# Kernel tuning notes

Measured on AMD Instinct MI355X. Metric: run time of the kernel, lower is better.

Reference implementation:

```python
import jax, jax.numpy as jnp
import numpy as np

B, S, HID, H, DH = 4, 1024, 1024, 16, 64
MAX_REL = 16
SCALE = 1.0 / (DH ** 0.5)


def _rel_bias(emb, seq_len):
    # Shaw-style relative position bias: emb is [2*MAX_REL+1, DH]
    pos = jnp.arange(seq_len)
    dist = jnp.clip(pos[None, :] - pos[:, None], -MAX_REL, MAX_REL) + MAX_REL
    return emb[dist]  # [S, S, DH]


def setup_inputs() -> dict:
    key = jax.random.key(0)
    ks = jax.random.split(key, 14)
    n = jax.random.normal
    w = 0.02
    return {
        "query": n(ks[0], (B, S, HID), dtype=jnp.float32),
        "key": n(ks[1], (B, S, HID), dtype=jnp.float32),
        "value": n(ks[2], (B, S, HID), dtype=jnp.float32),
        # per-head projection weights stacked over heads
        "Wq": n(ks[3], (H, HID, DH), dtype=jnp.float32) * w,
        "bq": n(ks[4], (H, DH), dtype=jnp.float32) * w,
        "Wk": n(ks[5], (H, HID, DH), dtype=jnp.float32) * w,
        "bk": n(ks[6], (H, DH), dtype=jnp.float32) * w,
        "Wv": n(ks[7], (H, HID, DH), dtype=jnp.float32) * w,
        "bv": n(ks[8], (H, DH), dtype=jnp.float32) * w,
        # relative-position embedding tables (shared across heads)
        "rel_k_emb": n(ks[9], (2 * MAX_REL + 1, DH), dtype=jnp.float32) * w,
        "rel_v_emb": n(ks[10], (2 * MAX_REL + 1, DH), dtype=jnp.float32) * w,
        # output projection fc: Linear(hidden, hidden)
        "fc_W": n(ks[11], (HID, HID), dtype=jnp.float32) * w,
        "fc_b": n(ks[12], (HID,), dtype=jnp.float32) * w,
    }


def reference(query, key, value, Wq, bq, Wk, bk, Wv, bv, rel_k_emb, rel_v_emb, fc_W, fc_b):
    # per-head projections, all heads batched: [B, H, S, DH]
    q = jnp.einsum('bsd,hde->bhse', query, Wq) + bq[None, :, None, :]
    k = jnp.einsum('bsd,hde->bhse', key, Wk) + bk[None, :, None, :]
    v = jnp.einsum('bsd,hde->bhse', value, Wv) + bv[None, :, None, :]

    k_bias = _rel_bias(rel_k_emb, S)  # [S, S, DH]
    v_bias = _rel_bias(rel_v_emb, S)  # [S, S, DH]

    # scores: QK^T plus relative-position key bias term
    scores = jnp.einsum('bhqe,bhke->bhqk', q, k)
    scores = scores + jnp.einsum('bhqe,qke->bhqk', q, k_bias)
    attn = jax.nn.softmax(scores * SCALE, axis=-1)  # [B, H, S, S]

    # values: A V plus relative-position value bias term
    out = jnp.einsum('bhqk,bhke->bhqe', attn, v)
    out = out + jnp.einsum('bhqk,qke->bhqe', attn, v_bias)

    # concat heads -> [B, S, HID], then fc
    out = out.transpose(0, 2, 1, 3).reshape(B, S, HID)
    return out @ fc_W.T + fc_b
```

## Files before the change

kernel.cpp:

```cpp
#include <hip/hip_runtime.h>
#include <stdint.h>

#define B_ 4
#define S_ 1024
#define HID_ 1024
#define H_ 16
#define DH_ 64
#define NDIST 33
#define SCALE_ 0.125f

typedef unsigned short u16;
typedef __attribute__((ext_vector_type(8))) short short8;
typedef __attribute__((ext_vector_type(4))) float floatx4;

static __device__ __forceinline__ float bf2f(u16 u) {
  union { unsigned int i; float f; } v; v.i = ((unsigned int)u) << 16; return v.f;
}
static __device__ __forceinline__ u16 f2bf(float x) {
  union { float f; unsigned int i; } v; v.f = x;
  return (u16)((v.i + 0x7FFFu + ((v.i >> 16) & 1u)) >> 16);
}
static __device__ __forceinline__ floatx4 mfma_bf16(short8 a, short8 b, floatx4 c) {
  return __builtin_amdgcn_mfma_f32_16x16x32_bf16(a, b, c, 0, 0, 0);
}
static __device__ __forceinline__ void gload_lds16(const void* g, void* l) {
  __builtin_amdgcn_global_load_lds(
      (const __attribute__((address_space(1))) unsigned int*)g,
      (__attribute__((address_space(3))) unsigned int*)l, 16, 0, 0);
}

#define OFF_BQ   0
#define OFF_BK   1024
#define OFF_BV   2048
#define OFF_RELK 3072
#define OFF_RELV 5184
#define OFF_FCW  7296
#define OFF_FCB  1055872
#define CONV_TOT 1056896

struct SrcPtrs { const void* p[7]; };

__global__ __launch_bounds__(256) void detect_kernel(const u16* __restrict__ q,
                                                     int* __restrict__ flag) {
  __shared__ float red[256];
  float m = 0.f;
  for (int i = threadIdx.x; i < 8192; i += 256) {
    float v = fabsf(bf2f(q[2 * i]));
    m = fmaxf(m, (v < 1e30f) ? v : 1e20f);
  }
  red[threadIdx.x] = m;
  __syncthreads();
  for (int s = 128; s > 0; s >>= 1) {
    if (threadIdx.x < (unsigned)s) red[threadIdx.x] = fmaxf(red[threadIdx.x], red[threadIdx.x + s]);
    __syncthreads();
  }
  if (threadIdx.x == 0) *flag = (red[0] > 1e4f) ? 1 : 0;
}

__global__ __launch_bounds__(256) void convert_kernel(SrcPtrs srcs,
                                                      const int* __restrict__ flag,
                                                      u16* __restrict__ dst) {
  constexpr int segsz[7] = {1024,1024,1024,2112,2112,1048576,1024};
  constexpr int cumE[7]  = {OFF_BQ,OFF_BK,OFF_BV,OFF_RELK,OFF_RELV,OFF_FCW,OFF_FCB};
  constexpr int cumB[8]  = {0,1,2,3,6,9,1033,1034};
  const int bid = blockIdx.x;
  int t = 0;
  #pragma unroll
  for (int i = 1; i < 7; ++i) if (bid >= cumB[i]) t = i;
  const int chunk = (bid - cumB[t]) * 1024 + threadIdx.x * 4;
  if (chunk >= segsz[t]) return;
  __align__(8) u16 o[4];
  if (*flag) {
    const float* s = (const float*)srcs.p[t];
    float4 v = *(const float4*)(s + chunk);
    o[0] = f2bf(v.x); o[1] = f2bf(v.y); o[2] = f2bf(v.z); o[3] = f2bf(v.w);
  } else {
    const u16* s = (const u16*)srcs.p[t];
    *(uint2*)o = *(const uint2*)(s + chunk);
  }
  *(uint2*)(dst + cumE[t] + chunk) = *(const uint2*)o;
}

__global__ __launch_bounds__(256) void wtrans_kernel(
    const void* __restrict__ Wq, const void* __restrict__ Wk, const void* __restrict__ Wv,
    const int* __restrict__ flag, u16* __restrict__ wt)
{
  const int dt = blockIdx.x, h = blockIdx.y, z = blockIdx.z;
  const void* W = (z == 0) ? Wq : (z == 1) ? Wk : Wv;
  const int tid = threadIdx.x;
  const int isf = *flag;
  __shared__ __align__(16) u16 t_l[64 * 72];

  #pragma unroll
  for (int i = 0; i < 2; ++i) {
    int g = tid + 256 * i;
    int d = g & 63, e8 = (g >> 6) * 8;
    size_t off = ((size_t)h * HID_ + dt * 64 + d) * DH_ + e8;
    __align__(16) u16 tmp[8];
    if (isf) {
      const float* Wf = (const float*)W + off;
      float4 v0 = *(const float4*)Wf;
      float4 v1 = *(const float4*)(Wf + 4);
      tmp[0]=f2bf(v0.x); tmp[1]=f2bf(v0.y); tmp[2]=f2bf(v0.z); tmp[3]=f2bf(v0.w);
      tmp[4]=f2bf(v1.x); tmp[5]=f2bf(v1.y); tmp[6]=f2bf(v1.z); tmp[7]=f2bf(v1.w);
    } else {
      *(uint4*)tmp = *(const uint4*)((const u16*)W + off);
    }
    #pragma unroll
    for (int j = 0; j < 8; ++j) {
      int e = e8 + j;
      t_l[e * 72 + (((d >> 3) ^ (e & 7)) << 3) + (d & 7)] = tmp[j];
    }
  }
  __syncthreads();
  {
    int e = tid >> 2, c0 = (tid & 3) * 2;
    u16* dst = wt + ((size_t)(z * H_ + h) * DH_ + e) * HID_ + dt * 64;
    uint4 x0 = *(const uint4*)(t_l + e * 72 + (((c0    ) ^ (e & 7)) << 3));
    uint4 x1 = *(const uint4*)(t_l + e * 72 + (((c0 + 1) ^ (e & 7)) << 3));
    *(uint4*)(dst + c0 * 8)     = x0;
    *(uint4*)(dst + c0 * 8 + 8) = x1;
  }
}

__global__ __launch_bounds__(256) void proj_kernel(
    const void* __restrict__ qin, const void* __restrict__ kin, const void* __restrict__ vin,
    const u16* __restrict__ wt, const u16* __restrict__ conv,
    const int* __restrict__ flag,
    u16* __restrict__ qo, u16* __restrict__ ko, u16* __restrict__ vo)
{
  const int z = blockIdx.z;
  const void* A   = (z == 0) ? qin : (z == 1) ? kin : vin;
  const u16* Wz   = wt + (size_t)z * (H_ * DH_ * HID_);
  const u16* bias = conv + ((z == 0) ? OFF_BQ : (z == 1) ? OFF_BK : OFF_BV);
  u16*       O    = (z == 0) ? qo : (z == 1) ? ko : vo;
  const int rt = blockIdx.x, ct = blockIdx.y;
  const int tid = threadIdx.x, lane = tid & 63, w = tid >> 6, quad = lane >> 4, l16 = lane & 15;
  const int isf = *flag;

  __shared__ __align__(16) u16 a_l[128 * 32];
  __shared__ __align__(16) u16 b_l[128 * 32];

  floatx4 acc[4][4];
  #pragma unroll
  for (int i = 0; i < 4; ++i)
    #pragma unroll
    for (int j = 0; j < 4; ++j) acc[i][j] = (floatx4){0.f,0.f,0.f,0.f};

  const int mq = (w & 1) * 64, nq = (w >> 1) * 64;

  for (int kk = 0; kk < 32; ++kk) {
    __syncthreads();
    #pragma unroll
    for (int i = 0; i < 2; ++i) {
      int idx = tid + 256 * i;
      int row = idx >> 2, c8 = (idx & 3) * 8;
      if (isf) {
        const float* Af = (const float*)A + (size_t)(rt * 128 + row) * HID_ + kk * 32 + c8;
        float4 v0 = *(const float4*)Af;
        float4 v1 = *(const float4*)(Af + 4);
        __align__(16) u16 tmp[8] = {f2bf(v0.x),f2bf(v0.y),f2bf(v0.z),f2bf(v0.w),
                                    f2bf(v1.x),f2bf(v1.y),f2bf(v1.z),f2bf(v1.w)};
        *(uint4*)(a_l + row * 32 + c8) = *(const uint4*)tmp;
      } else {
        *(uint4*)(a_l + row * 32 + c8) =
            *(const uint4*)((const u16*)A + (size_t)(rt * 128 + row) * HID_ + kk * 32 + c8);
      }
      gload_lds16(Wz + (size_t)(ct * 128 + row) * HID_ + kk * 32 + c8,
                  b_l + ((size_t)(w * 64 + i * 256)) * 8);
    }
    __syncthreads();
    short8 af[4], bfr[4];
    #pragma unroll
    for (int i = 0; i < 4; ++i) {
      af[i]  = *(const short8*)(a_l + (mq + i * 16 + l16) * 32 + quad * 8);
      bfr[i] = *(const short8*)(b_l + (nq + i * 16 + l16) * 32 + quad * 8);
    }
    #pragma unroll
    for (int i = 0; i < 4; ++i)
      #pragma unroll
      for (int j = 0; j < 4; ++j)
        acc[i][j] = mfma_bf16(af[i], bfr[j], acc[i][j]);
  }

  #pragma unroll
  for (int j = 0; j < 4; ++j) {
    int col = ct * 128 + nq + j * 16 + l16;
    int hh = col >> 6, e = col & 63;
    float bb = bf2f(bias[hh * 64 + e]);
    #pragma unroll
    for (int i = 0; i < 4; ++i) {
      #pragma unroll
      for (int r = 0; r < 4; ++r) {
        int m = rt * 128 + mq + i * 16 + quad * 4 + r;
        int bidx = m >> 10, srow = m & 1023;
        O[(((size_t)(bidx * H_ + hh)) * S_ + srow) * DH_ + e] = f2bf(acc[i][j][r] + bb);
      }
    }
  }
}

__global__ __launch_bounds__(256, 4) void attn_kernel(
    const u16* __restrict__ Q, const u16* __restrict__ K, const u16* __restrict__ V,
    const u16* __restrict__ conv, u16* __restrict__ Ox)
{
  const int bid = blockIdx.x + 16 * (blockIdx.y + 16 * blockIdx.z);
  const int nid = (bid & 7) * 128 + (bid >> 3);
  const int qt = nid & 15, h = (nid >> 4) & 15, b = nid >> 8;

  const int tid = threadIdx.x;
  const int lane = tid & 63, w = tid >> 6, quad = lane >> 4, l16 = lane & 15;
  const size_t base = ((size_t)(b * H_ + h)) * S_ * DH_;

  __shared__ __align__(16) char smem[40320];
  u16*   p_l    = (u16*)(smem);
  u16*   q_l    = p_l;
  u16*   k_l    = (u16*)(smem + 9216);
  u16*   vt_l   = (u16*)(smem + 18432);
  u16*   rq_l   = (u16*)(smem + 27648);
  float* bucket = (float*)(smem + 31872);
  u16*   rkb    = (u16*)(smem + 31872);

  #pragma unroll
  for (int i = 0; i < 2; ++i) {
    int idx = tid + 256 * i;
    int row = idx >> 3, c8 = (idx & 7) * 8;
    *(uint4*)(q_l + row * 72 + c8) =
        *(const uint4*)(Q + base + (size_t)(qt * 64 + row) * DH_ + c8);
  }
  const u16* relk = conv + OFF_RELK;
  for (int idx = tid; idx < 48 * 8; idx += 256) {
    int row = idx >> 3, c8 = (idx & 7) * 8;
    uint4 v = make_uint4(0, 0, 0, 0);
    if (row < NDIST) v = *(const uint4*)(relk + row * 64 + c8);
    *(uint4*)(rkb + row * 72 + c8) = v;
  }
  __syncthreads();

  const int m0 = w * 16;
  short8 qa0 = *(const short8*)(q_l + (m0 + l16) * 72 + quad * 8);
  short8 qa1 = *(const short8*)(q_l + (m0 + l16) * 72 + 32 + quad * 8);

  floatx4 c_d0 = {0.f,0.f,0.f,0.f}, c_d32 = {0.f,0.f,0.f,0.f};
  #pragma unroll
  for (int t3 = 0; t3 < 3; ++t3) {
    floatx4 c = {0.f,0.f,0.f,0.f};
    c = mfma_bf16(qa0, *(const short8*)(rkb + (t3 * 16 + l16) * 72 + quad * 8), c);
    c = mfma_bf16(qa1, *(const short8*)(rkb + (t3 * 16 + l16) * 72 + 32 + quad * 8), c);
    if (t3 == 0) c_d0 = c;
    if (t3 == 2) c_d32 = c;
    int d = t3 * 16 + l16;
    if (d < NDIST) {
      #pragma unroll
      for (int r = 0; r < 4; ++r) rq_l[(m0 + quad * 4 + r) * 33 + d] = f2bf(c[r]);
    }
  }
  float rqs_lo[4], rqs_hi[4];
  #pragma unroll
  for (int r = 0; r < 4; ++r) {
    rqs_lo[r] = bf2f(f2bf(__shfl(c_d0[r],  lane & 48, 64))) * SCALE_;
    rqs_hi[r] = bf2f(f2bf(__shfl(c_d32[r], lane & 48, 64))) * SCALE_;
  }
  __syncthreads();
  for (int idx = tid; idx < 64 * 33; idx += 256) bucket[idx] = 0.f;

  floatx4 o[4], oi = {0.f,0.f,0.f,0.f};
  #pragma unroll
  for (int t = 0; t < 4; ++t) o[t] = (floatx4){0.f,0.f,0.f,0.f};

  for (int kt = 0; kt < 16; ++kt) {
    __syncthreads();
    #pragma unroll
    for (int i = 0; i < 2; ++i) {
      int idx = tid + 256 * i;
      int row = idx >> 3, c8 = (idx & 7) * 8;
      *(uint4*)(k_l + row * 72 + c8) =
          *(const uint4*)(K + base + (size_t)(kt * 64 + row) * DH_ + c8);
    }
    {
      int kcol = lane;
      #pragma unroll
      for (int ph = 0; ph < 2; ++ph) {
        int e8 = w * 16 + ph * 8;
        uint4 vv = *(const uint4*)(V + base + (size_t)(kt * 64 + kcol) * DH_ + e8);
        const u16* t8 = (const u16*)&vv;
        #pragma unroll
        for (int j = 0; j < 8; ++j) {
          vt_l[(e8 + j) * 72 + kcol] = t8[j];
        }
      }
    }
    __syncthreads();

    const int dkt = kt - qt;
    const bool near = (dkt >= -1) && (dkt <= 1);

    #pragma unroll
    for (int t = 0; t < 4; ++t) {
      floatx4 s = {0.f,0.f,0.f,0.f};
      s = mfma_bf16(qa0, *(const short8*)(k_l + (t * 16 + l16) * 72 + quad * 8), s);
      s = mfma_bf16(qa1, *(const short8*)(k_l + (t * 16 + l16) * 72 + 32 + quad * 8), s);
      int kcol = t * 16 + l16;
      if (near) {
        #pragma unroll
        for (int r = 0; r < 4; ++r) {
          int m = m0 + quad * 4 + r;
          int delta = (kt * 64 + kcol) - (qt * 64 + m);
          int dist = (delta < -16 ? -16 : (delta > 16 ? 16 : delta)) + 16;
          float logit = (s[r] + bf2f(rq_l[m * 33 + dist])) * SCALE_;
          u16 pu = f2bf(__expf(fminf(logit, 30.f)));
          p_l[m * 72 + kcol] = pu;
          float pv = bf2f(pu);
          float vhi = (dist == 32) ? pv : 0.f;
          float vlo = (dist == 0) ? pv : 0.f;
          #pragma unroll
          for (int off2 = 1; off2 < 16; off2 <<= 1) {
            vhi += __shfl_xor(vhi, off2, 16);
            vlo += __shfl_xor(vlo, off2, 16);
          }
          if (l16 == 0) {
            if (vhi != 0.f) atomicAdd(&bucket[m * 33 + 32], vhi);
            if (vlo != 0.f) atomicAdd(&bucket[m * 33 + 0], vlo);
          }
          if (dist > 0 && dist < 32) atomicAdd(&bucket[m * 33 + dist], pv);
        }
      } else {
        #pragma unroll
        for (int r = 0; r < 4; ++r) {
          int m = m0 + quad * 4 + r;
          float logit = fmaf(s[r], SCALE_, (dkt < 0) ? rqs_lo[r] : rqs_hi[r]);
          u16 pu = f2bf(__expf(fminf(logit, 30.f)));
          p_l[m * 72 + kcol] = pu;
        }
      }
    }

    u16 iv = ((l16 == 0 && dkt <= -2) || (l16 == 1 && dkt >= 2)) ? (u16)0x3F80 : (u16)0;
    short8 ib;
    #pragma unroll
    for (int j = 0; j < 8; ++j) ib[j] = (short)iv;
    short8 pa0 = *(const short8*)(p_l + (m0 + l16) * 72 + quad * 8);
    short8 pa1 = *(const short8*)(p_l + (m0 + l16) * 72 + 32 + quad * 8);
    oi = mfma_bf16(pa0, ib, oi);
    oi = mfma_bf16(pa1, ib, oi);
    #pragma unroll
    for (int t = 0; t < 4; ++t) {
      int e = t * 16 + l16;
      short8 vb0 = *(const short8*)(vt_l + e * 72 + quad * 8);
      short8 vb1 = *(const short8*)(vt_l + e * 72 + 32 + quad * 8);
      o[t] = mfma_bf16(pa0, vb0, o[t]);
      o[t] = mfma_bf16(pa1, vb1, o[t]);
    }
  }

  __syncthreads();
  if (l16 == 0) {
    #pragma unroll
    for (int r = 0; r < 4; ++r) bucket[(m0 + quad * 4 + r) * 33 + 0] += oi[r];
  } else if (l16 == 1) {
    #pragma unroll
    for (int r = 0; r < 4; ++r) bucket[(m0 + quad * 4 + r) * 33 + 32] += oi[r];
  }
  __syncthreads();

  u16* rvT = k_l;
  u16* Bf  = p_l;
  for (int idx = tid; idx < 576; idx += 256) {
    ((uint4*)rvT)[idx] = make_uint4(0, 0, 0, 0);
    ((uint4*)Bf)[idx]  = make_uint4(0, 0, 0, 0);
  }
  __syncthreads();
  const u16* relv = conv + OFF_RELV;
  for (int idx = tid; idx < NDIST * 64; idx += 256) {
    int d = idx >> 6, e = idx & 63;
    rvT[e * 72 + d] = relv[idx];
  }
  for (int idx = tid; idx < 64 * NDIST; idx += 256) {
    int m = idx / NDIST, d = idx - m * NDIST;
    Bf[m * 72 + d] = f2bf(bucket[m * 33 + d]);
  }
  __syncthreads();

  short8 ba0 = *(const short8*)(Bf + (m0 + l16) * 72 + quad * 8);
  short8 ba1 = *(const short8*)(Bf + (m0 + l16) * 72 + 32 + quad * 8);
  #pragma unroll
  for (int t = 0; t < 4; ++t) {
    short8 rb0 = *(const short8*)(rvT + (t * 16 + l16) * 72 + quad * 8);
    short8 rb1 = *(const short8*)(rvT + (t * 16 + l16) * 72 + 32 + quad * 8);
    o[t] = mfma_bf16(ba0, rb0, o[t]);
    o[t] = mfma_bf16(ba1, rb1, o[t]);
  }

  float rl[4];
  #pragma unroll
  for (int r = 0; r < 4; ++r) {
    int m = m0 + quad * 4 + r;
    float s = 0.f;
    #pragma unroll
    for (int d = 0; d < NDIST; ++d) s += bucket[m * 33 + d];
    rl[r] = 1.f / s;
  }

  #pragma unroll
  for (int t = 0; t < 4; ++t) {
    int e = t * 16 + l16;
    #pragma unroll
    for (int r = 0; r < 4; ++r) {
      int srow = qt * 64 + m0 + quad * 4 + r;
      Ox[((size_t)(b * S_ + srow)) * HID_ + h * 64 + e] = f2bf(o[t][r] * rl[r]);
    }
  }
}

__global__ __launch_bounds__(256) void fc_kernel(
    const u16* __restrict__ X, const u16* __restrict__ conv,
    const int* __restrict__ flag, void* __restrict__ outv)
{
  const u16* Wf  = conv + OFF_FCW;
  const u16* bfc = conv + OFF_FCB;
  const int rt = blockIdx.x, ct = blockIdx.y;
  const int tid = threadIdx.x, lane = tid & 63, w = tid >> 6, quad = lane >> 4, l16 = lane & 15;
  const int isf = *flag;

  __shared__ __align__(16) u16 a_l[128 * 32];
  __shared__ __align__(16) u16 b_l[128 * 32];

  floatx4 acc[4][4];
  #pragma unroll
  for (int i = 0; i < 4; ++i)
    #pragma unroll
    for (int j = 0; j < 4; ++j) acc[i][j] = (floatx4){0.f,0.f,0.f,0.f};

  const int mq = (w & 1) * 64, nq = (w >> 1) * 64;

  for (int kk = 0; kk < 32; ++kk) {
    __syncthreads();
    #pragma unroll
    for (int i = 0; i < 2; ++i) {
      int idx = tid + 256 * i;
      int row = idx >> 2, c8 = (idx & 3) * 8;
      gload_lds16(X + (size_t)(rt * 128 + row) * HID_ + kk * 32 + c8,
                  a_l + ((size_t)(w * 64 + i * 256)) * 8);
      gload_lds16(Wf + (size_t)(ct * 128 + row) * HID_ + kk * 32 + c8,
                  b_l + ((size_t)(w * 64 + i * 256)) * 8);
    }
    __syncthreads();
    short8 af[4], bfr[4];
    #pragma unroll
    for (int i = 0; i < 4; ++i) {
      af[i]  = *(const short8*)(a_l + (mq + i * 16 + l16) * 32 + quad * 8);
      bfr[i] = *(const short8*)(b_l + (nq + i * 16 + l16) * 32 + quad * 8);
    }
    #pragma unroll
    for (int i = 0; i < 4; ++i)
      #pragma unroll
      for (int j = 0; j < 4; ++j)
        acc[i][j] = mfma_bf16(af[i], bfr[j], acc[i][j]);
  }

  #pragma unroll
  for (int j = 0; j < 4; ++j) {
    int col = ct * 128 + nq + j * 16 + l16;
    float bb = bf2f(bfc[col]);
    #pragma unroll
    for (int i = 0; i < 4; ++i) {
      #pragma unroll
      for (int r = 0; r < 4; ++r) {
        int m = rt * 128 + mq + i * 16 + quad * 4 + r;
        float val = acc[i][j][r] + bb;
        size_t idx = (size_t)m * HID_ + col;
        if (isf) ((float*)outv)[idx] = val;
        else     ((u16*)outv)[idx]   = f2bf(val);
      }
    }
  }
}

extern "C" void kernel_launch(void* const* d_in, const int* in_sizes, int n_in,
                              void* d_out, int out_size, void* d_ws, size_t ws_size,
                              hipStream_t stream) {
  int* flag = (int*)d_ws;
  u16* conv = (u16*)((char*)d_ws + 16);
  u16* wt   = conv + CONV_TOT;
  u16* qw   = wt + 3145728;
  u16* kw   = qw + 4194304;
  u16* vw   = kw + 4194304;
  u16* xw   = vw + 4194304;

  detect_kernel<<<1, 256, 0, stream>>>((const u16*)d_in[0], flag);

  SrcPtrs sp;
  sp.p[0] = d_in[4];  sp.p[1] = d_in[6];  sp.p[2] = d_in[8];
  sp.p[3] = d_in[9];  sp.p[4] = d_in[10]; sp.p[5] = d_in[11]; sp.p[6] = d_in[12];
  convert_kernel<<<1034, 256, 0, stream>>>(sp, flag, conv);

  wtrans_kernel<<<dim3(16, 16, 3), 256, 0, stream>>>(d_in[3], d_in[5], d_in[7], flag, wt);
  proj_kernel<<<dim3(32, 8, 3), 256, 0, stream>>>(d_in[0], d_in[1], d_in[2],
                                                  wt, conv, flag, qw, kw, vw);
  attn_kernel<<<dim3(16, 16, 4), 256, 0, stream>>>(qw, kw, vw, conv, xw);
  fc_kernel<<<dim3(32, 8), 256, 0, stream>>>(xw, conv, flag, (u16*)d_out);
}
```

Baseline: 310.9 us.

## Pre-convert QKV inputs to bf16, double-buffer LDS with swizzle in GEMMs

Adds a separate kernel that converts the fp32 query/key/value activations to bf16 into workspace, so the projection GEMM can load its A operand with direct global-to-LDS async loads. Both the projection and fc GEMMs now double-buffer the LDS tiles, prefetching the next k-slice while computing the current one, and drop one barrier per iteration. They also apply an XOR swizzle to LDS columns to reduce bank conflicts, with a 3-blocks-per-CU occupancy hint. The cost is an extra full pass over the inputs through memory, plus doubled LDS per block. The converted-input buffers alias the xw buffer, which is only written later by attention.

```diff
diff --git a/kernel.cpp b/kernel.cpp
--- a/kernel.cpp
+++ b/kernel.cpp
@@ -79,6 +79,31 @@
     *(uint2*)o = *(const uint2*)(s + chunk);
   }
   *(uint2*)(dst + cumE[t] + chunk) = *(const uint2*)o;
+}
+
+__global__ __launch_bounds__(256) void qkvconv_kernel(
+    const void* __restrict__ qin, const void* __restrict__ kin,
+    const void* __restrict__ vin, const int* __restrict__ flag,
+    u16* __restrict__ qc, u16* __restrict__ kc, u16* __restrict__ vc)
+{
+  const int isf = *flag;
+  const int total = 3 * (4096 * 1024 / 8);
+  for (int g = blockIdx.x * 256 + threadIdx.x; g < total; g += gridDim.x * 256) {
+    const int z = g >> 19;
+    const int off = (g & 524287) * 8;
+    const void* src = (z == 0) ? qin : (z == 1) ? kin : vin;
+    u16* dst = (z == 0) ? qc : (z == 1) ? kc : vc;
+    if (isf) {
+      const float* s = (const float*)src + off;
+      float4 v0 = *(const float4*)s;
+      float4 v1 = *(const float4*)(s + 4);
+      __align__(16) u16 tmp[8] = {f2bf(v0.x),f2bf(v0.y),f2bf(v0.z),f2bf(v0.w),
+                                  f2bf(v1.x),f2bf(v1.y),f2bf(v1.z),f2bf(v1.w)};
+      *(uint4*)(dst + off) = *(const uint4*)tmp;
+    } else {
+      *(uint4*)(dst + off) = *(const uint4*)((const u16*)src + off);
+    }
+  }
 }
 
 __global__ __launch_bounds__(256) void wtrans_kernel(
@@ -123,23 +148,21 @@
   }
 }
 
-__global__ __launch_bounds__(256) void proj_kernel(
-    const void* __restrict__ qin, const void* __restrict__ kin, const void* __restrict__ vin,
+__global__ __launch_bounds__(256, 3) void proj_kernel(
+    const u16* __restrict__ qc, const u16* __restrict__ kc, const u16* __restrict__ vc,
     const u16* __restrict__ wt, const u16* __restrict__ conv,
-    const int* __restrict__ flag,
     u16* __restrict__ qo, u16* __restrict__ ko, u16* __restrict__ vo)
 {
   const int z = blockIdx.z;
-  const void* A   = (z == 0) ? qin : (z == 1) ? kin : vin;
+  const u16* A    = (z == 0) ? qc : (z == 1) ? kc : vc;
   const u16* Wz   = wt + (size_t)z * (H_ * DH_ * HID_);
   const u16* bias = conv + ((z == 0) ? OFF_BQ : (z == 1) ? OFF_BK : OFF_BV);
   u16*       O    = (z == 0) ? qo : (z == 1) ? ko : vo;
   const int rt = blockIdx.x, ct = blockIdx.y;
   const int tid = threadIdx.x, lane = tid & 63, w = tid >> 6, quad = lane >> 4, l16 = lane & 15;
-  const int isf = *flag;
-
-  __shared__ __align__(16) u16 a_l[128 * 32];
-  __shared__ __align__(16) u16 b_l[128 * 32];
+
+  __shared__ __align__(16) u16 a_l[2][128 * 32];
+  __shared__ __align__(16) u16 b_l[2][128 * 32];
 
   floatx4 acc[4][4];
   #pragma unroll
@@ -148,39 +171,39 @@
     for (int j = 0; j < 4; ++j) acc[i][j] = (floatx4){0.f,0.f,0.f,0.f};
 
   const int mq = (w & 1) * 64, nq = (w >> 1) * 64;
-
+  const int u = (lane & 3) ^ ((lane >> 3) & 3);
+  const int cs = (quad ^ ((l16 >> 1) & 3)) * 8;
+
+  auto STAGE = [&](int bu, int kk) {
+    #pragma unroll
+    for (int i = 0; i < 2; ++i) {
+      int row = (tid + 256 * i) >> 2;
+      gload_lds16(A  + (size_t)(rt * 128 + row) * HID_ + kk * 32 + u * 8,
+                  a_l[bu] + (w * 64 + i * 256) * 8);
+      gload_lds16(Wz + (size_t)(ct * 128 + row) * HID_ + kk * 32 + u * 8,
+                  b_l[bu] + (w * 64 + i * 256) * 8);
+    }
+  };
+
+  STAGE(0, 0);
+  int cur = 0;
   for (int kk = 0; kk < 32; ++kk) {
     __syncthreads();
-    #pragma unroll
-    for (int i = 0; i < 2; ++i) {
-      int idx = tid + 256 * i;
-      int row = idx >> 2, c8 = (idx & 3) * 8;
-      if (isf) {
-        const float* Af = (const float*)A + (size_t)(rt * 128 + row) * HID_ + kk * 32 + c8;
-        float4 v0 = *(const float4*)Af;
-        float4 v1 = *(const float4*)(Af + 4);
-        __align__(16) u16 tmp[8] = {f2bf(v0.x),f2bf(v0.y),f2bf(v0.z),f2bf(v0.w),
-                                    f2bf(v1.x),f2bf(v1.y),f2bf(v1.z),f2bf(v1.w)};
-        *(uint4*)(a_l + row * 32 + c8) = *(const uint4*)tmp;
-      } else {
-        *(uint4*)(a_l + row * 32 + c8) =
-            *(const uint4*)((const u16*)A + (size_t)(rt * 128 + row) * HID_ + kk * 32 + c8);
-      }
-      gload_lds16(Wz + (size_t)(ct * 128 + row) * HID_ + kk * 32 + c8,
-                  b_l + ((size_t)(w * 64 + i * 256)) * 8);
-    }
-    __syncthreads();
+    if (kk + 1 < 32) STAGE(cur ^ 1, kk + 1);
+    const u16* ab = a_l[cur];
+    const u16* bb = b_l[cur];
     short8 af[4], bfr[4];
     #pragma unroll
     for (int i = 0; i < 4; ++i) {
-      af[i]  = *(const short8*)(a_l + (mq + i * 16 + l16) * 32 + quad * 8);
-      bfr[i] = *(const short8*)(b_l + (nq + i * 16 + l16) * 32 + quad * 8);
+      af[i]  = *(const short8*)(ab + (mq + i * 16 + l16) * 32 + cs);
+      bfr[i] = *(const short8*)(bb + (nq + i * 16 + l16) * 32 + cs);
     }
     #pragma unroll
     for (int i = 0; i < 4; ++i)
       #pragma unroll
       for (int j = 0; j < 4; ++j)
         acc[i][j] = mfma_bf16(af[i], bfr[j], acc[i][j]);
+    cur ^= 1;
   }
 
   #pragma unroll
@@ -412,7 +435,7 @@
   }
 }
 
-__global__ __launch_bounds__(256) void fc_kernel(
+__global__ __launch_bounds__(256, 3) void fc_kernel(
     const u16* __restrict__ X, const u16* __restrict__ conv,
     const int* __restrict__ flag, void* __restrict__ outv)
 {
@@ -422,8 +445,8 @@
   const int tid = threadIdx.x, lane = tid & 63, w = tid >> 6, quad = lane >> 4, l16 = lane & 15;
   const int isf = *flag;
 
-  __shared__ __align__(16) u16 a_l[128 * 32];
-  __shared__ __align__(16) u16 b_l[128 * 32];
+  __shared__ __align__(16) u16 a_l[2][128 * 32];
+  __shared__ __align__(16) u16 b_l[2][128 * 32];
 
   floatx4 acc[4][4];
   #pragma unroll
@@ -432,30 +455,39 @@
     for (int j = 0; j < 4; ++j) acc[i][j] = (floatx4){0.f,0.f,0.f,0.f};
 
   const int mq = (w & 1) * 64, nq = (w >> 1) * 64;
-
+  const int u = (lane & 3) ^ ((lane >> 3) & 3);
+  const int cs = (quad ^ ((l16 >> 1) & 3)) * 8;
+
+  auto STAGE = [&](int bu, int kk) {
+    #pragma unroll
+    for (int i = 0; i < 2; ++i) {
+      int row = (tid + 256 * i) >> 2;
+      gload_lds16(X  + (size_t)(rt * 128 + row) * HID_ + kk * 32 + u * 8,
+                  a_l[bu] + (w * 64 + i * 256) * 8);
+      gload_lds16(Wf + (size_t)(ct * 128 + row) * HID_ + kk * 32 + u * 8,
+                  b_l[bu] + (w * 64 + i * 256) * 8);
+    }
+  };
+
+  STAGE(0, 0);
+  int cur = 0;
   for (int kk = 0; kk < 32; ++kk) {
     __syncthreads();
-    #pragma unroll
-    for (int i = 0; i < 2; ++i) {
-      int idx = tid + 256 * i;
-      int row = idx >> 2, c8 = (idx & 3) * 8;
-      gload_lds16(X + (size_t)(rt * 128 + row) * HID_ + kk * 32 + c8,
-                  a_l + ((size_t)(w * 64 + i * 256)) * 8);
-      gload_lds16(Wf + (size_t)(ct * 128 + row) * HID_ + kk * 32 + c8,
-                  b_l + ((size_t)(w * 64 + i * 256)) * 8);
-    }
-    __syncthreads();
+    if (kk + 1 < 32) STAGE(cur ^ 1, kk + 1);
+    const u16* ab = a_l[cur];
+    const u16* bb = b_l[cur];
     short8 af[4], bfr[4];
     #pragma unroll
     for (int i = 0; i < 4; ++i) {
-      af[i]  = *(const short8*)(a_l + (mq + i * 16 + l16) * 32 + quad * 8);
-      bfr[i] = *(const short8*)(b_l + (nq + i * 16 + l16) * 32 + quad * 8);
+      af[i]  = *(const short8*)(ab + (mq + i * 16 + l16) * 32 + cs);
+      bfr[i] = *(const short8*)(bb + (nq + i * 16 + l16) * 32 + cs);
     }
     #pragma unroll
     for (int i = 0; i < 4; ++i)
       #pragma unroll
       for (int j = 0; j < 4; ++j)
         acc[i][j] = mfma_bf16(af[i], bfr[j], acc[i][j]);
+    cur ^= 1;
   }
 
   #pragma unroll
@@ -486,6 +518,9 @@
   u16* kw   = qw + 4194304;
   u16* vw   = kw + 4194304;
   u16* xw   = vw + 4194304;
+  u16* qc   = xw;
+  u16* kc   = xw + 4194304;
+  u16* vc   = kc + 4194304;
 
   detect_kernel<<<1, 256, 0, stream>>>((const u16*)d_in[0], flag);
 
@@ -493,10 +528,10 @@
   sp.p[0] = d_in[4];  sp.p[1] = d_in[6];  sp.p[2] = d_in[8];
   sp.p[3] = d_in[9];  sp.p[4] = d_in[10]; sp.p[5] = d_in[11]; sp.p[6] = d_in[12];
   convert_kernel<<<1034, 256, 0, stream>>>(sp, flag, conv);
+  qkvconv_kernel<<<2048, 256, 0, stream>>>(d_in[0], d_in[1], d_in[2], flag, qc, kc, vc);
 
   wtrans_kernel<<<dim3(16, 16, 3), 256, 0, stream>>>(d_in[3], d_in[5], d_in[7], flag, wt);
-  proj_kernel<<<dim3(32, 8, 3), 256, 0, stream>>>(d_in[0], d_in[1], d_in[2],
-                                                  wt, conv, flag, qw, kw, vw);
+  proj_kernel<<<dim3(32, 8, 3), 256, 0, stream>>>(qc, kc, vc, wt, conv, qw, kw, vw);
   attn_kernel<<<dim3(16, 16, 4), 256, 0, stream>>>(qw, kw, vw, conv, xw);
   fc_kernel<<<dim3(32, 8), 256, 0, stream>>>(xw, conv, flag, (u16*)d_out);
 }
```

New measurement: 295.0 us. 1.05x faster.
